# Performance work log

Measured on AMD Instinct MI355X. Metric: run time of the kernel, lower is better.

## Reference

```python
import jax, jax.numpy as jnp
import numpy as np

EPS = 0.0  # GINConv eps

def _gin_conv(x, edge_index, W1, b1, W2, b2, n_nodes):
    # GINConv: mlp((1+eps)*x + sum_{j in N(i)} x_j)
    src, dst = edge_index[0], edge_index[1]
    agg = jax.ops.segment_sum(x[src], dst, num_segments=n_nodes)  # [N, d]
    h = (1.0 + EPS) * x + agg
    h = jax.nn.relu(h @ W1 + b1)  # Linear -> Identity(BN off) -> ReLU
    return h @ W2 + b2            # second Linear


def setup_inputs() -> dict:
    key = jax.random.key(0)
    ks = jax.random.split(key, 10)
    N, E = 50000, 600000
    d_in, d_hid, d_out = 128, 256, 128
    x = jax.random.normal(ks[0], (N, d_in), dtype=jnp.float32)
    edge_index = jax.random.randint(ks[1], (2, E), 0, N, dtype=jnp.int64)

    def lin(k, fan_in, fan_out):
        bound = 1.0 / np.sqrt(fan_in)
        kw, kb = jax.random.split(k)
        W = jax.random.uniform(kw, (fan_in, fan_out), jnp.float32, -bound, bound)
        b = jax.random.uniform(kb, (fan_out,), jnp.float32, -bound, bound)
        return W, b

    W1a, b1a = lin(ks[2], d_in, d_hid)   # conv0 mlp: 128->256
    W2a, b2a = lin(ks[3], d_hid, d_hid)  # conv0 mlp: 256->256
    W1b, b1b = lin(ks[4], d_hid, d_hid)  # conv1 mlp: 256->256
    W2b, b2b = lin(ks[5], d_hid, d_out)  # conv1 mlp: 256->128
    return {"x": x, "W1a": W1a, "b1a": b1a, "W2a": W2a, "b2a": b2a,
            "W1b": W1b, "b1b": b1b, "W2b": W2b, "b2b": b2b,
            "edge_index": edge_index}


def reference(x, W1a, b1a, W2a, b2a, W1b, b1b, W2b, b2b, edge_index):
    n_nodes = x.shape[0]
    # layer 0: GINConv -> relu (use_bn=False; dropout is identity in eval)
    h = _gin_conv(x, edge_index, W1a, b1a, W2a, b2a, n_nodes)
    h = jax.nn.relu(h)
    # final GINConv (no activation after, per forward())
    return _gin_conv(h, edge_index, W1b, b1b, W2b, b2b, n_nodes)
```

## Files before the change

### kernel.cpp

```cpp
#include <hip/hip_runtime.h>


typedef __bf16 bf16x8 __attribute__((ext_vector_type(8)));
typedef float f32x4 __attribute__((ext_vector_type(4)));
typedef float f32x2 __attribute__((ext_vector_type(2)));
typedef unsigned short u16x4 __attribute__((ext_vector_type(4)));
typedef unsigned short u16x8 __attribute__((ext_vector_type(8)));
typedef unsigned int uint32;
typedef uint32 u32x4 __attribute__((ext_vector_type(4)));

__device__ __forceinline__ unsigned short f2bf(float f) {
  uint32 u = __builtin_bit_cast(uint32, f);
  u += 0x7FFFu + ((u >> 16) & 1u);
  return (unsigned short)(u >> 16);
}
__device__ __forceinline__ f32x2 bfpair(uint32 w) {
  f32x2 r;
  r.x = __builtin_bit_cast(float, w << 16);
  r.y = __builtin_bit_cast(float, w & 0xFFFF0000u);
  return r;
}

#define G2L16(gp, lp)                                                        \
  __builtin_amdgcn_global_load_lds(                                          \
      (const __attribute__((address_space(1))) void*)(gp),                   \
      (__attribute__((address_space(3))) void*)(lp), 16, 0, 0)

__global__ void hist(const int* __restrict__ eidx, int* __restrict__ deg, int E) {
  int e = blockIdx.x * blockDim.x + threadIdx.x;
  if (e < E) atomicAdd(&deg[eidx[e + E]], 1);
}

__global__ __launch_bounds__(256) void scan_all(
    const int* __restrict__ deg, int* __restrict__ offs, int* __restrict__ pos,
    int* __restrict__ aggr, int* __restrict__ incl, int* __restrict__ flg,
    int Nn, int nb) {
  __shared__ int sm[256];
  __shared__ int s_prefix;
  const int t = threadIdx.x;
  const int b = blockIdx.x;
  const int i = b * 256 + t;
  int v = (i < Nn) ? deg[i] : 0;
  sm[t] = v;
  __syncthreads();
#pragma unroll
  for (int off = 1; off < 256; off <<= 1) {
    int add = (t >= off) ? sm[t - off] : 0;
    __syncthreads();
    sm[t] += add;
    __syncthreads();
  }
  if (t == 255) {
    atomicExch(&aggr[b], sm[255]);
    atomicExch(&flg[b], 1);
  }
  if (b == 0) {
    for (int j = t; j < nb; j += 256)
      while (atomicAdd(&flg[j], 0) == 0) __builtin_amdgcn_s_sleep(1);
    __syncthreads();
    int a = (t < nb) ? atomicAdd(&aggr[t], 0) : 0;
    __shared__ int sb[256];
    sb[t] = a;
    __syncthreads();
#pragma unroll
    for (int off = 1; off < 256; off <<= 1) {
      int add = (t >= off) ? sb[t - off] : 0;
      __syncthreads();
      sb[t] += add;
      __syncthreads();
    }
    if (t < nb) atomicExch(&incl[t], sb[t]);
    __syncthreads();
    if (t == 0) atomicExch(&flg[nb], 1);
    if (t == 0) s_prefix = 0;
  } else {
    if (t == 0) {
      while (atomicAdd(&flg[nb], 0) == 0) __builtin_amdgcn_s_sleep(8);
      s_prefix = atomicAdd(&incl[b - 1], 0);
    }
  }
  __syncthreads();
  int ex = s_prefix + sm[t] - v;
  if (i < Nn) {
    offs[i] = ex;
    pos[i] = ex;
    if (i == Nn - 1) offs[Nn] = ex + v;
  }
}

__global__ void fill_csr(const int* __restrict__ eidx, int* __restrict__ pos,
                         int* __restrict__ esrc, int E) {
  int e = blockIdx.x * blockDim.x + threadIdx.x;
  if (e < E) {
    int s = eidx[e];
    int d = eidx[e + E];
    int p = atomicAdd(&pos[d], 1);
    esrc[p] = s;
  }
}

__global__ __launch_bounds__(256) void prep(
    int* __restrict__ zp, int zn,
    const float* __restrict__ x, unsigned short* __restrict__ xb, long long n4,
    const float* __restrict__ W1a, const float* __restrict__ W2a,
    const float* __restrict__ W1b, const float* __restrict__ W2b,
    unsigned short* __restrict__ w1t, unsigned short* __restrict__ w2t,
    unsigned short* __restrict__ w3t, unsigned short* __restrict__ w4t) {
  int zb = (zn + 255) >> 8;
  int b = blockIdx.x;
  int t = threadIdx.x;
  if (b < zb) {
    int i = b * 256 + t;
    if (i < zn) zp[i] = 0;
  } else if (b < zb + 768) {
    int i = (b - zb) * 256 + t;
    const float* W;
    unsigned short* WT;
    int K, N, j;
    if (i < 32768) {
      W = W1a; WT = w1t; K = 128; N = 256; j = i;
    } else if (i < 98304) {
      W = W2a; WT = w2t; K = 256; N = 256; j = i - 32768;
    } else if (i < 163840) {
      W = W1b; WT = w3t; K = 256; N = 256; j = i - 98304;
    } else {
      W = W2b; WT = w4t; K = 256; N = 128; j = i - 163840;
    }
    int k = j / N, n = j - k * N;
    WT[n * K + k] = f2bf(W[j]);
  } else {
    long long i = (long long)(b - zb - 768) * 256 + t;
    long long stride = (long long)(gridDim.x - zb - 768) * 256;
    for (; i < n4; i += stride) {
      float4 v = ((const float4*)x)[i];
      u16x4 o;
      o.x = f2bf(v.x); o.y = f2bf(v.y); o.z = f2bf(v.z); o.w = f2bf(v.w);
      ((u16x4*)xb)[i] = o;
    }
  }
}

__global__ __launch_bounds__(256) void agg_bf16_128(
    unsigned short* __restrict__ out, const unsigned short* __restrict__ xb,
    const int* __restrict__ offs, const int* __restrict__ esrc, int Nn) {
  int node = blockIdx.x * 4 + (threadIdx.x >> 6);
  if (node >= Nn) return;
  int lane = threadIdx.x & 63;
  int grp = lane >> 4, l16 = lane & 15;
  int beg = offs[node], end = offs[node + 1];
  int total = end - beg + 1;
  const unsigned short* xp = xb + l16 * 8;
  f32x2 acc[4] = {};
  for (int j0 = 0; j0 < total; j0 += 16) {
#pragma unroll
    for (int u = 0; u < 4; ++u) {
      int j = j0 + u * 4 + grp;
      int rv = esrc[beg + j - (j > 0)];
      long long row = (j > 0 && j < total) ? rv : node;
      float sel = (j < total) ? 1.f : 0.f;
      f32x2 fsel = {sel, sel};
      u32x4 w = *(const u32x4*)(xp + row * 128);
#pragma unroll
      for (int k = 0; k < 4; ++k) acc[k] += bfpair(w[k]) * fsel;
    }
  }
  float s[8];
#pragma unroll
  for (int k = 0; k < 4; ++k) { s[2 * k] = acc[k].x; s[2 * k + 1] = acc[k].y; }
#pragma unroll
  for (int k = 0; k < 8; ++k) s[k] += __shfl_xor(s[k], 16);
#pragma unroll
  for (int k = 0; k < 8; ++k) s[k] += __shfl_xor(s[k], 32);
  if (grp == 0) {
    u16x8 o;
#pragma unroll
    for (int k = 0; k < 8; ++k) o[k] = f2bf(s[k]);
    *(u16x8*)(out + (long long)node * 128 + l16 * 8) = o;
  }
}

__global__ __launch_bounds__(256) void agg_bf16_256(
    unsigned short* __restrict__ out, const unsigned short* __restrict__ h,
    const int* __restrict__ offs, const int* __restrict__ esrc, int Nn) {
  int node = blockIdx.x * 4 + (threadIdx.x >> 6);
  if (node >= Nn) return;
  int lane = threadIdx.x & 63;
  int grp = lane >> 5, l32 = lane & 31;
  int beg = offs[node], end = offs[node + 1];
  int total = end - beg + 1;
  const unsigned short* hp = h + l32 * 8;
  f32x2 acc[4] = {};
  for (int j0 = 0; j0 < total; j0 += 16) {
#pragma unroll
    for (int u = 0; u < 8; ++u) {
      int j = j0 + u * 2 + grp;
      int rv = esrc[beg + j - (j > 0)];
      long long row = (j > 0 && j < total) ? rv : node;
      float sel = (j < total) ? 1.f : 0.f;
      f32x2 fsel = {sel, sel};
      u32x4 w = *(const u32x4*)(hp + row * 256);
#pragma unroll
      for (int k = 0; k < 4; ++k) acc[k] += bfpair(w[k]) * fsel;
    }
  }
  float s[8];
#pragma unroll
  for (int k = 0; k < 4; ++k) { s[2 * k] = acc[k].x; s[2 * k + 1] = acc[k].y; }
#pragma unroll
  for (int k = 0; k < 8; ++k) s[k] += __shfl_xor(s[k], 32);
  if (grp == 0) {
    u16x8 o;
#pragma unroll
    for (int k = 0; k < 8; ++k) o[k] = f2bf(s[k]);
    *(u16x8*)(out + (long long)node * 256 + l32 * 8) = o;
  }
}

template <int K1, int N2, bool OUT_BF16>
__global__ __launch_bounds__(256) void fused_mlp(
    const unsigned short* __restrict__ A,
    const unsigned short* __restrict__ BT1, const float* __restrict__ b1,
    const unsigned short* __restrict__ BT2, const float* __restrict__ b2,
    void* __restrict__ Cout, int M) {
  __shared__ unsigned short As[64 * 32];
  __shared__ unsigned short Bs[256 * 32];
  __shared__ unsigned short Ts[64 * 264];
  const int tid = threadIdx.x;
  const int wave = tid >> 6, lane = tid & 63;
  const int quad = lane >> 4, l16 = lane & 15;
  const int rowBase = blockIdx.x * 64;
  const int r16 = lane >> 2;
  const int kq = lane & 3;

  long long arow = min(rowBase + wave * 16 + r16, M - 1);
  const unsigned short* ga = A + arow * K1 + kq * 8;
  const unsigned short* gb = BT1 + (long long)(wave * 64 + r16) * K1 + kq * 8;
  unsigned short* la = As + wave * 16 * 32;
  f32x4 acc[4][4] = {};
  for (int k0 = 0; k0 < K1; k0 += 32) {
    G2L16(ga, la);
    ga += 32;
#pragma unroll
    for (int c = 0; c < 4; ++c)
      G2L16(gb + (long long)(16 * c) * K1, Bs + (wave * 64 + 16 * c) * 32);
    gb += 32;
    __syncthreads();
    bf16x8 af[4], bfr[4];
#pragma unroll
    for (int mi = 0; mi < 4; ++mi)
      af[mi] = *(const bf16x8*)(As + (mi * 16 + l16) * 32 + quad * 8);
#pragma unroll
    for (int ni = 0; ni < 4; ++ni)
      bfr[ni] = *(const bf16x8*)(Bs + (wave * 64 + ni * 16 + l16) * 32 + quad * 8);
#pragma unroll
    for (int mi = 0; mi < 4; ++mi)
#pragma unroll
      for (int ni = 0; ni < 4; ++ni)
        acc[mi][ni] = __builtin_amdgcn_mfma_f32_16x16x32_bf16(
            af[mi], bfr[ni], acc[mi][ni], 0, 0, 0);
    __syncthreads();
  }
#pragma unroll
  for (int ni = 0; ni < 4; ++ni) {
    int col = wave * 64 + ni * 16 + l16;
    float bv = b1[col];
#pragma unroll
    for (int mi = 0; mi < 4; ++mi)
#pragma unroll
      for (int r = 0; r < 4; ++r) {
        int row = mi * 16 + quad * 4 + r;
        Ts[row * 264 + col] = f2bf(fmaxf(acc[mi][ni][r] + bv, 0.f));
      }
  }
  __syncthreads();

  constexpr int NI2 = N2 / 64;
  const int wcol = wave * (N2 / 4);
  const unsigned short* gb2 = BT2 + (long long)(wcol + r16) * 256 + kq * 8;
  f32x4 acc2[4][NI2] = {};
  for (int k2 = 0; k2 < 256; k2 += 32) {
#pragma unroll
    for (int c = 0; c < NI2; ++c)
      G2L16(gb2 + (long long)(16 * c) * 256, Bs + (wcol + 16 * c) * 32);
    gb2 += 32;
    __syncthreads();
    bf16x8 af[4], bfr[NI2];
#pragma unroll
    for (int mi = 0; mi < 4; ++mi)
      af[mi] = *(const bf16x8*)(Ts + (mi * 16 + l16) * 264 + k2 + quad * 8);
#pragma unroll
    for (int ni = 0; ni < NI2; ++ni)
      bfr[ni] = *(const bf16x8*)(Bs + (wcol + ni * 16 + l16) * 32 + quad * 8);
#pragma unroll
    for (int mi = 0; mi < 4; ++mi)
#pragma unroll
      for (int ni = 0; ni < NI2; ++ni)
        acc2[mi][ni] = __builtin_amdgcn_mfma_f32_16x16x32_bf16(
            af[mi], bfr[ni], acc2[mi][ni], 0, 0, 0);
    __syncthreads();
  }
#pragma unroll
  for (int ni = 0; ni < NI2; ++ni) {
    int col = wcol + ni * 16 + l16;
    float bv = b2[col];
#pragma unroll
    for (int mi = 0; mi < 4; ++mi)
#pragma unroll
      for (int r = 0; r < 4; ++r) {
        int row = rowBase + mi * 16 + quad * 4 + r;
        if (row < M) {
          float o = acc2[mi][ni][r] + bv;
          if (OUT_BF16)
            ((unsigned short*)Cout)[(long long)row * N2 + col] = f2bf(fmaxf(o, 0.f));
          else
            ((float*)Cout)[(long long)row * N2 + col] = o;
        }
      }
  }
}

extern "C" void kernel_launch(void* const* d_in, const int* in_sizes, int n_in,
                              void* d_out, int out_size, void* d_ws, size_t ws_size,
                              hipStream_t stream) {
  const float* x   = (const float*)d_in[0];
  const float* W1a = (const float*)d_in[1];
  const float* b1a = (const float*)d_in[2];
  const float* W2a = (const float*)d_in[3];
  const float* b2a = (const float*)d_in[4];
  const float* W1b = (const float*)d_in[5];
  const float* b1b = (const float*)d_in[6];
  const float* W2b = (const float*)d_in[7];
  const float* b2b = (const float*)d_in[8];
  const int*   ei  = (const int*)d_in[9];

  const int Nn = in_sizes[0] / 128;
  const int E  = in_sizes[9] / 2;
  float* out = (float*)d_out;

  const int nb = (Nn + 255) / 256;

  unsigned short* h   = (unsigned short*)d_ws;
  unsigned short* g0  = h  + (size_t)Nn * 256;
  unsigned short* g1  = g0 + (size_t)Nn * 128;
  unsigned short* xb  = g1 + (size_t)Nn * 256;
  unsigned short* w1t = xb + (size_t)Nn * 128;
  unsigned short* w2t = w1t + 256 * 128;
  unsigned short* w3t = w2t + 256 * 256;
  unsigned short* w4t = w3t + 256 * 256;
  int* deg  = (int*)(w4t + 128 * 256);
  int* flg  = deg + Nn;
  int* aggr = flg + nb + 1;
  int* incl = aggr + nb;
  int* offs = incl + nb;
  int* pos  = offs + Nn + 1;
  int* esrc = pos + Nn;

  dim3 blk(256);
  int zn = Nn + nb + 1;
  int zb = (zn + 255) / 256;

  prep<<<zb + 768 + 2048, blk, 0, stream>>>(deg, zn, x, xb,
                                            (long long)Nn * 128 / 4,
                                            W1a, W2a, W1b, W2b,
                                            w1t, w2t, w3t, w4t);
  hist<<<(E + 255) / 256, blk, 0, stream>>>(ei, deg, E);
  scan_all<<<nb, blk, 0, stream>>>(deg, offs, pos, aggr, incl, flg, Nn, nb);
  fill_csr<<<(E + 255) / 256, blk, 0, stream>>>(ei, pos, esrc, E);

  int aggBlocks = (Nn + 3) / 4;
  int mlpBlocks = (Nn + 63) / 64;

  agg_bf16_128<<<aggBlocks, blk, 0, stream>>>(g0, xb, offs, esrc, Nn);
  fused_mlp<128, 256, true><<<mlpBlocks, blk, 0, stream>>>(
      g0, w1t, b1a, w2t, b2a, h, Nn);
  agg_bf16_256<<<aggBlocks, blk, 0, stream>>>(g1, h, offs, esrc, Nn);
  fused_mlp<256, 128, false><<<mlpBlocks, blk, 0, stream>>>(
      g1, w3t, b1b, w4t, b2b, out, Nn);
}
```

Before: 290.9 us.

## Assign one lane group per node in aggregation and swizzle MLP shared-memory tiles

The two aggregation kernels become one templated grid-stride kernel. Each group of 16 or 32 lanes owns a whole node, walks its edges eight at a time with batched index loads, and no longer needs the cross-lane shuffle reduction. The fused MLP also applies an XOR swizzle to the k-quarter offset of the A and B shared-memory tiles, to reduce LDS bank conflicts on the fragment reads. The per-node mapping can leave lanes idle when node degrees vary, and the fixed 2048-block grid may not match occupancy.

```diff
diff --git a/kernel.cpp b/kernel.cpp
--- a/kernel.cpp
+++ b/kernel.cpp
@@ -140,79 +140,57 @@
   }
 }
 
-__global__ __launch_bounds__(256) void agg_bf16_128(
-    unsigned short* __restrict__ out, const unsigned short* __restrict__ xb,
+template <int GRP>
+__global__ __launch_bounds__(256) void agg_gather(
+    unsigned short* __restrict__ out, const unsigned short* __restrict__ src,
     const int* __restrict__ offs, const int* __restrict__ esrc, int Nn) {
-  int node = blockIdx.x * 4 + (threadIdx.x >> 6);
-  if (node >= Nn) return;
-  int lane = threadIdx.x & 63;
-  int grp = lane >> 4, l16 = lane & 15;
-  int beg = offs[node], end = offs[node + 1];
-  int total = end - beg + 1;
-  const unsigned short* xp = xb + l16 * 8;
-  f32x2 acc[4] = {};
-  for (int j0 = 0; j0 < total; j0 += 16) {
-#pragma unroll
-    for (int u = 0; u < 4; ++u) {
-      int j = j0 + u * 4 + grp;
-      int rv = esrc[beg + j - (j > 0)];
-      long long row = (j > 0 && j < total) ? rv : node;
-      float sel = (j < total) ? 1.f : 0.f;
-      f32x2 fsel = {sel, sel};
-      u32x4 w = *(const u32x4*)(xp + row * 128);
-#pragma unroll
-      for (int k = 0; k < 4; ++k) acc[k] += bfpair(w[k]) * fsel;
-    }
-  }
-  float s[8];
-#pragma unroll
-  for (int k = 0; k < 4; ++k) { s[2 * k] = acc[k].x; s[2 * k + 1] = acc[k].y; }
-#pragma unroll
-  for (int k = 0; k < 8; ++k) s[k] += __shfl_xor(s[k], 16);
-#pragma unroll
-  for (int k = 0; k < 8; ++k) s[k] += __shfl_xor(s[k], 32);
-  if (grp == 0) {
+  constexpr int RS = GRP * 8;
+  constexpr int GPB = 256 / GRP;
+  const int gid = threadIdx.x / GRP;
+  const int gl  = threadIdx.x % GRP;
+  const unsigned short* sp = src + gl * 8;
+  const int stride = gridDim.x * GPB;
+  for (int node = blockIdx.x * GPB + gid; node < Nn; node += stride) {
+    const int beg = offs[node];
+    const int deg = offs[node + 1] - beg;
+    f32x2 acc[4];
+    {
+      u32x4 w = *(const u32x4*)(sp + node * RS);
+#pragma unroll
+      for (int k = 0; k < 4; ++k) acc[k] = bfpair(w[k]);
+    }
+    int j = 0;
+    for (; j + 8 <= deg; j += 8) {
+      int idx[8];
+#pragma unroll
+      for (int u = 0; u < 8; ++u) idx[u] = esrc[beg + j + u];
+#pragma unroll
+      for (int u = 0; u < 8; ++u) {
+        u32x4 w = *(const u32x4*)(sp + idx[u] * RS);
+#pragma unroll
+        for (int k = 0; k < 4; ++k) acc[k] += bfpair(w[k]);
+      }
+    }
+    if (j < deg) {
+#pragma unroll
+      for (int u = 0; u < 8; ++u) {
+        int jj = j + u;
+        int e = beg + (jj < deg ? jj : deg - 1);
+        float sel = (jj < deg) ? 1.f : 0.f;
+        f32x2 fs = {sel, sel};
+        int rv = esrc[e];
+        u32x4 w = *(const u32x4*)(sp + rv * RS);
+#pragma unroll
+        for (int k = 0; k < 4; ++k) acc[k] += bfpair(w[k]) * fs;
+      }
+    }
     u16x8 o;
 #pragma unroll
-    for (int k = 0; k < 8; ++k) o[k] = f2bf(s[k]);
-    *(u16x8*)(out + (long long)node * 128 + l16 * 8) = o;
-  }
-}
-
-__global__ __launch_bounds__(256) void agg_bf16_256(
-    unsigned short* __restrict__ out, const unsigned short* __restrict__ h,
-    const int* __restrict__ offs, const int* __restrict__ esrc, int Nn) {
-  int node = blockIdx.x * 4 + (threadIdx.x >> 6);
-  if (node >= Nn) return;
-  int lane = threadIdx.x & 63;
-  int grp = lane >> 5, l32 = lane & 31;
-  int beg = offs[node], end = offs[node + 1];
-  int total = end - beg + 1;
-  const unsigned short* hp = h + l32 * 8;
-  f32x2 acc[4] = {};
-  for (int j0 = 0; j0 < total; j0 += 16) {
-#pragma unroll
-    for (int u = 0; u < 8; ++u) {
-      int j = j0 + u * 2 + grp;
-      int rv = esrc[beg + j - (j > 0)];
-      long long row = (j > 0 && j < total) ? rv : node;
-      float sel = (j < total) ? 1.f : 0.f;
-      f32x2 fsel = {sel, sel};
-      u32x4 w = *(const u32x4*)(hp + row * 256);
-#pragma unroll
-      for (int k = 0; k < 4; ++k) acc[k] += bfpair(w[k]) * fsel;
-    }
-  }
-  float s[8];
-#pragma unroll
-  for (int k = 0; k < 4; ++k) { s[2 * k] = acc[k].x; s[2 * k + 1] = acc[k].y; }
-#pragma unroll
-  for (int k = 0; k < 8; ++k) s[k] += __shfl_xor(s[k], 32);
-  if (grp == 0) {
-    u16x8 o;
-#pragma unroll
-    for (int k = 0; k < 8; ++k) o[k] = f2bf(s[k]);
-    *(u16x8*)(out + (long long)node * 256 + l32 * 8) = o;
+    for (int k = 0; k < 4; ++k) {
+      o[2 * k] = f2bf(acc[k].x);
+      o[2 * k + 1] = f2bf(acc[k].y);
+    }
+    *(u16x8*)(out + (size_t)node * RS + gl * 8) = o;
   }
 }
 
@@ -231,10 +209,12 @@
   const int rowBase = blockIdx.x * 64;
   const int r16 = lane >> 2;
   const int kq = lane & 3;
+  const int kqs = kq ^ ((r16 >> 1) & 3);
+  const int sq = (quad ^ ((l16 >> 1) & 3)) * 8;
 
   long long arow = min(rowBase + wave * 16 + r16, M - 1);
-  const unsigned short* ga = A + arow * K1 + kq * 8;
-  const unsigned short* gb = BT1 + (long long)(wave * 64 + r16) * K1 + kq * 8;
+  const unsigned short* ga = A + arow * K1 + kqs * 8;
+  const unsigned short* gb = BT1 + (long long)(wave * 64 + r16) * K1 + kqs * 8;
   unsigned short* la = As + wave * 16 * 32;
   f32x4 acc[4][4] = {};
   for (int k0 = 0; k0 < K1; k0 += 32) {
@@ -248,10 +228,10 @@
     bf16x8 af[4], bfr[4];
 #pragma unroll
     for (int mi = 0; mi < 4; ++mi)
-      af[mi] = *(const bf16x8*)(As + (mi * 16 + l16) * 32 + quad * 8);
+      af[mi] = *(const bf16x8*)(As + (mi * 16 + l16) * 32 + sq);
 #pragma unroll
     for (int ni = 0; ni < 4; ++ni)
-      bfr[ni] = *(const bf16x8*)(Bs + (wave * 64 + ni * 16 + l16) * 32 + quad * 8);
+      bfr[ni] = *(const bf16x8*)(Bs + (wave * 64 + ni * 16 + l16) * 32 + sq);
 #pragma unroll
     for (int mi = 0; mi < 4; ++mi)
 #pragma unroll
@@ -276,7 +256,7 @@
 
   constexpr int NI2 = N2 / 64;
   const int wcol = wave * (N2 / 4);
-  const unsigned short* gb2 = BT2 + (long long)(wcol + r16) * 256 + kq * 8;
+  const unsigned short* gb2 = BT2 + (long long)(wcol + r16) * 256 + kqs * 8;
   f32x4 acc2[4][NI2] = {};
   for (int k2 = 0; k2 < 256; k2 += 32) {
 #pragma unroll
@@ -290,7 +270,7 @@
       af[mi] = *(const bf16x8*)(Ts + (mi * 16 + l16) * 264 + k2 + quad * 8);
 #pragma unroll
     for (int ni = 0; ni < NI2; ++ni)
-      bfr[ni] = *(const bf16x8*)(Bs + (wcol + ni * 16 + l16) * 32 + quad * 8);
+      bfr[ni] = *(const bf16x8*)(Bs + (wcol + ni * 16 + l16) * 32 + sq);
 #pragma unroll
     for (int mi = 0; mi < 4; ++mi)
 #pragma unroll
@@ -367,13 +347,12 @@
   scan_all<<<nb, blk, 0, stream>>>(deg, offs, pos, aggr, incl, flg, Nn, nb);
   fill_csr<<<(E + 255) / 256, blk, 0, stream>>>(ei, pos, esrc, E);
 
-  int aggBlocks = (Nn + 3) / 4;
   int mlpBlocks = (Nn + 63) / 64;
 
-  agg_bf16_128<<<aggBlocks, blk, 0, stream>>>(g0, xb, offs, esrc, Nn);
+  agg_gather<16><<<2048, blk, 0, stream>>>(g0, xb, offs, esrc, Nn);
   fused_mlp<128, 256, true><<<mlpBlocks, blk, 0, stream>>>(
       g0, w1t, b1a, w2t, b2a, h, Nn);
-  agg_bf16_256<<<aggBlocks, blk, 0, stream>>>(g1, h, offs, esrc, Nn);
+  agg_gather<32><<<2048, blk, 0, stream>>>(g1, h, offs, esrc, Nn);
   fused_mlp<256, 128, false><<<mlpBlocks, blk, 0, stream>>>(
       g1, w3t, b1b, w4t, b2b, out, Nn);
 }
```

New measurement: 292.4 us. No clear change (+0.5%).
